# Kernel tuning notes

Hardware: AMD Instinct MI355X
Metric: run time of the kernel (lower is better)

## Reference

```python
import jax, jax.numpy as jnp
import numpy as np

# dims: O=1 templates/chains, L=384 residues, d_pair=d_bias=128, 4 heads x 32
O, L, DP, DB, H, DH = 1, 384, 128, 128, 4, 32
SCALING = 1.0 / np.sqrt(DH)


def _ln(x, g, b):
    # torch nn.LayerNorm over last dim, eps=1e-5, biased variance
    m = jnp.mean(x, axis=-1, keepdims=True)
    v = jnp.mean((x - m) ** 2, axis=-1, keepdims=True)
    return (x - m) * jax.lax.rsqrt(v + 1e-5) * g + b


def setup_inputs() -> dict:
    key = jax.random.key(0)
    ks = jax.random.split(key, 9)

    def w(k, shape, s=0.02):
        return (jax.random.normal(k, shape) * s).astype(jnp.float32)

    return {
        "pair": jax.random.normal(ks[0], (O, L, L, DP), dtype=jnp.float32),
        "bias": jax.random.normal(ks[1], (O, L, L, DB), dtype=jnp.float32),
        "ln_pair_g": jnp.ones((DP,), jnp.float32),
        "ln_pair_b": jnp.zeros((DP,), jnp.float32),
        "ln_bias_g": jnp.ones((DB,), jnp.float32),
        "ln_bias_b": jnp.zeros((DB,), jnp.float32),
        "Wq": w(ks[2], (H * DH, DP)),  # torch Linear weight layout (out, in)
        "Wk": w(ks[3], (H * DH, DP)),
        "Wv": w(ks[4], (H * DH, DP)),
        "Wb": w(ks[5], (H, DB)),
        "Wg": w(ks[6], (H * DH, DP)),
        "bg": jnp.ones((H * DH,), jnp.float32),
        "Wo": w(ks[7], (DP, H * DH)),
        "bo": w(ks[8], (DP,)),
    }


def reference(pair, bias, ln_pair_g, ln_pair_b, ln_bias_g, ln_bias_b,
              Wq, Wk, Wv, Wb, Wg, bg, Wo, bo):
    # is_row=True: swap the two L axes so attention runs along rows
    p = jnp.transpose(pair, (0, 2, 1, 3))   # [O, L, L, DP]
    bsrc = jnp.transpose(bias, (0, 2, 1, 3))  # [O, L, L, DB]

    p = _ln(p, ln_pair_g, ln_pair_b)
    bsrc = _ln(bsrc, ln_bias_g, ln_bias_b)

    q = (p @ Wq.T).reshape(O, L, L, H, DH) * SCALING
    k = (p @ Wk.T).reshape(O, L, L, H, DH) / L
    v = (p @ Wv.T).reshape(O, L, L, H, DH)
    b = bsrc @ Wb.T                         # [O, L, L, H] pairwise bias
    gate = jax.nn.sigmoid(p @ Wg.T + bg)    # [O, L, L, H*DH]

    # attention scores contracted over the non-attended axial dim n and head dim k
    attn = jnp.einsum('bnihk,bnjhk->bijh', q, k) + b
    attn = jax.nn.softmax(attn, axis=2)     # softmax over j (torch dim=-2)

    out = jnp.einsum('bijh,bnjhd->bnihd', attn, v).reshape(O, L, L, H * DH)
    out = (gate * out) @ Wo.T + bo          # [O, L, L, DP]
    return jnp.transpose(out, (0, 2, 1, 3))  # undo is_row permute
```

## Files before the change

kernel.cpp:

```cpp
#include <hip/hip_runtime.h>
#include <hip/hip_bf16.h>

#define L_DIM 384
#define DPC 128
#define NH 4
#define DHD 32
#define HD 128
#define NROWS (L_DIM*L_DIM)
#define NSPLIT 16

typedef __hip_bfloat16 bf16;
typedef __attribute__((ext_vector_type(8))) short bf8_t;
typedef __attribute__((ext_vector_type(4))) short bf4_t;
typedef __attribute__((ext_vector_type(4))) float f4_t;

__device__ __forceinline__ float bf2f(bf16 x){ return __bfloat162float(x); }
__device__ __forceinline__ bf16 f2bf(float x){ return __float2bfloat16(x); }

union bfu8 { bf8_t v; bf16 h[8]; };

__global__ __launch_bounds__(256) void k_prep(
    const float* __restrict__ Wq, const float* __restrict__ Wk, const float* __restrict__ Wv,
    const float* __restrict__ Wg, const float* __restrict__ Wo,
    bf16* __restrict__ Wqp, bf16* __restrict__ Wkp, bf16* __restrict__ Wvp,
    bf16* __restrict__ Wgp, bf16* __restrict__ Wop)
{
  const int o = blockIdx.x * 256 + threadIdx.x;
  const int j = o & 7, lane = (o >> 3) & 63, ks = (o >> 9) & 3, nt = o >> 11;
  const int src = (nt*16 + (lane & 15))*DPC + ks*32 + (lane >> 4)*8 + j;
  Wqp[o] = f2bf(Wq[src]);
  Wkp[o] = f2bf(Wk[src]);
  Wvp[o] = f2bf(Wv[src]);
  Wgp[o] = f2bf(Wg[src]);
  Wop[o] = f2bf(Wo[src]);
}

__global__ __launch_bounds__(256) void k_bias_proj(
    const float* __restrict__ bias, const float* __restrict__ lng, const float* __restrict__ lnb,
    const float* __restrict__ Wb, float* __restrict__ bscore)
{
  const int tid = threadIdx.x;
  const int wave = tid >> 6, lane = tid & 63;
  const int sub = lane >> 4, l16 = lane & 15, c = l16 * 8;
  const int t = blockIdx.x * 16 + wave * 4 + sub;
  const int j = t / L_DIM, i = t % L_DIM;

  const float4 ga = *(const float4*)&lng[c], gb = *(const float4*)&lng[c+4];
  const float4 ba = *(const float4*)&lnb[c], bb = *(const float4*)&lnb[c+4];
  const float4 xa = *(const float4*)&bias[(size_t)t * DPC + c];
  const float4 xb = *(const float4*)&bias[(size_t)t * DPC + c + 4];

  float s  = xa.x+xa.y+xa.z+xa.w + xb.x+xb.y+xb.z+xb.w;
  float ss = xa.x*xa.x+xa.y*xa.y+xa.z*xa.z+xa.w*xa.w
           + xb.x*xb.x+xb.y*xb.y+xb.z*xb.z+xb.w*xb.w;
  #pragma unroll
  for (int off = 8; off; off >>= 1) { s += __shfl_xor(s, off, 64); ss += __shfl_xor(ss, off, 64); }
  const float mean = s * (1.f/128.f);
  const float var  = ss * (1.f/128.f) - mean*mean;
  const float rstd = rsqrtf(var + 1e-5f);
  float y[8];
  y[0]=(xa.x-mean)*rstd*ga.x+ba.x; y[1]=(xa.y-mean)*rstd*ga.y+ba.y;
  y[2]=(xa.z-mean)*rstd*ga.z+ba.z; y[3]=(xa.w-mean)*rstd*ga.w+ba.w;
  y[4]=(xb.x-mean)*rstd*gb.x+bb.x; y[5]=(xb.y-mean)*rstd*gb.y+bb.y;
  y[6]=(xb.z-mean)*rstd*gb.z+bb.z; y[7]=(xb.w-mean)*rstd*gb.w+bb.w;

  float p[4];
  #pragma unroll
  for (int h = 0; h < 4; ++h) {
    const float4 wa = *(const float4*)&Wb[h*DPC + c];
    const float4 wb4 = *(const float4*)&Wb[h*DPC + c + 4];
    p[h] = y[0]*wa.x + y[1]*wa.y + y[2]*wa.z + y[3]*wa.w
         + y[4]*wb4.x + y[5]*wb4.y + y[6]*wb4.z + y[7]*wb4.w;
    #pragma unroll
    for (int off = 8; off; off >>= 1) p[h] += __shfl_xor(p[h], off, 64);
  }
  if (l16 == 0) {
    #pragma unroll
    for (int h = 0; h < 4; ++h)
      bscore[((size_t)h*L_DIM + i)*L_DIM + j] = p[h];
  }
}

__global__ __launch_bounds__(256) void k_pair_proj(
    const float* __restrict__ pair, const float* __restrict__ lng, const float* __restrict__ lnb,
    const bf16* __restrict__ Wqp, const bf16* __restrict__ Wkp, const bf16* __restrict__ Wvp,
    const bf16* __restrict__ Wgp, const float* __restrict__ bg,
    bf16* __restrict__ qf, bf16* __restrict__ kf, bf16* __restrict__ vf, bf16* __restrict__ gatef)
{
  __shared__ __align__(16) bf16 Sh[5120 + 3*4352];
  bf16* AsCT = Sh;
  bf16* Csq  = Sh + 5120;
  bf16* Csk  = Sh + 5120 + 4352;
  bf16* Csg  = Sh + 5120 + 2*4352;
  const int tid = threadIdx.x;
  const int wave = tid >> 6, lane = tid & 63;
  const int n = blockIdx.x / 12, i0 = (blockIdx.x % 12) * 32;
  const int m = lane & 15, q4 = lane >> 4;
  const int rt = wave >> 1, ch = wave & 1;

  {
    const int half = lane >> 5, l32 = lane & 31, c = l32 * 4;
    const float4 g4 = *(const float4*)&lng[c];
    const float4 b4 = *(const float4*)&lnb[c];
    float4 xv[4];
    #pragma unroll
    for (int rr = 0; rr < 4; ++rr) {
      int r = wave*8 + rr*2 + half;
      xv[rr] = *(const float4*)&pair[((size_t)(i0 + r)*L_DIM + n)*DPC + c];
    }
    #pragma unroll
    for (int rr = 0; rr < 4; ++rr) {
      int r = wave*8 + rr*2 + half;
      float s  = xv[rr].x + xv[rr].y + xv[rr].z + xv[rr].w;
      float ss = xv[rr].x*xv[rr].x + xv[rr].y*xv[rr].y + xv[rr].z*xv[rr].z + xv[rr].w*xv[rr].w;
      #pragma unroll
      for (int off = 16; off; off >>= 1) { s += __shfl_xor(s, off, 64); ss += __shfl_xor(ss, off, 64); }
      float mean = s * (1.f/128.f);
      float var  = ss * (1.f/128.f) - mean*mean;
      float rstd = rsqrtf(var + 1e-5f);
      union { bf16 h[4]; bf4_t v; } pk;
      pk.h[0] = f2bf((xv[rr].x-mean)*rstd*g4.x + b4.x);
      pk.h[1] = f2bf((xv[rr].y-mean)*rstd*g4.y + b4.y);
      pk.h[2] = f2bf((xv[rr].z-mean)*rstd*g4.z + b4.z);
      pk.h[3] = f2bf((xv[rr].w-mean)*rstd*g4.w + b4.w);
      *(bf4_t*)&AsCT[r*136 + c] = pk.v;
    }
  }
  __syncthreads();

  bf8_t afr[4];
  #pragma unroll
  for (int ks = 0; ks < 4; ++ks)
    afr[ks] = *(const bf8_t*)&AsCT[(rt*16 + m)*136 + ks*32 + q4*8];

  const bf16* W3[3] = {Wqp, Wkp, Wgp};
  bf16* C3[3] = {Csq, Csk, Csg};
  #pragma unroll
  for (int s3 = 0; s3 < 3; ++s3) {
    const bf16* Wp = W3[s3];
    bf16* Cs = C3[s3];
    #pragma unroll
    for (int ntl = 0; ntl < 4; ++ntl) {
      const int nt = ch*4 + ntl;
      f4_t acc = {0.f, 0.f, 0.f, 0.f};
      #pragma unroll
      for (int ks = 0; ks < 4; ++ks) {
        bf8_t bfr = *(const bf8_t*)&Wp[(nt*4 + ks)*512 + lane*8];
        acc = __builtin_amdgcn_mfma_f32_16x16x32_bf16(afr[ks], bfr, acc, 0, 0, 0);
      }
      const int col = nt*16 + m;
      const float bgv = (s3 == 2) ? bg[col] : 0.f;
      #pragma unroll
      for (int reg = 0; reg < 4; ++reg) {
        float v = acc[reg];
        if (s3 == 2) v = 1.f / (1.f + __expf(-(v + bgv)));
        Cs[(rt*16 + q4*4 + reg)*136 + col] = f2bf(v);
      }
    }
  }
  __syncthreads();

  #pragma unroll
  for (int ntl = 0; ntl < 4; ++ntl) {
    const int nt = ch*4 + ntl;
    f4_t acc = {0.f, 0.f, 0.f, 0.f};
    #pragma unroll
    for (int ks = 0; ks < 4; ++ks) {
      bf8_t bfr = *(const bf8_t*)&Wvp[(nt*4 + ks)*512 + lane*8];
      acc = __builtin_amdgcn_mfma_f32_16x16x32_bf16(afr[ks], bfr, acc, 0, 0, 0);
    }
    const int col = nt*16 + m;
    #pragma unroll
    for (int reg = 0; reg < 4; ++reg)
      AsCT[col*40 + rt*16 + q4*4 + reg] = f2bf(acc[reg]);
  }
  __syncthreads();

  #pragma unroll
  for (int it = 0; it < 2; ++it) {
    int u = tid + it*256;
    {
      int ln = u & 63, dt = (u >> 6) & 1, h = u >> 7;
      bf8_t val = *(const bf8_t*)&AsCT[(h*32 + dt*16 + (ln&15))*40 + (ln>>4)*8];
      size_t dst = ((((size_t)n*NH + h)*12 + (i0>>5))*2 + dt)*512 + (size_t)ln*8;
      *(bf8_t*)&vf[dst] = val;
    }
    {
      int Il = u >> 8, h = (u >> 6) & 3, ln = u & 63;
      int lidx = (Il*16 + (ln&15))*136 + h*32 + (ln>>4)*8;
      size_t dq = ((((size_t)n*NH + h)*24 + (i0>>4) + Il)*64 + ln)*8;
      *(bf8_t*)&qf[dq] = *(const bf8_t*)&Csq[lidx];
      *(bf8_t*)&kf[dq] = *(const bf8_t*)&Csk[lidx];
      size_t dg = ((((size_t)n*24 + (i0>>4) + Il)*NH + h)*64 + ln)*8;
      *(bf8_t*)&gatef[dg] = *(const bf8_t*)&Csg[lidx];
    }
  }
}

__global__ __launch_bounds__(256) void k_qk(
    const bf16* __restrict__ qf, const bf16* __restrict__ kf, float* __restrict__ Spart)
{
  const int tid = threadIdx.x, wave = tid >> 6, lane = tid & 63;
  const int m = lane & 15, q4 = lane >> 4;
  const int b = blockIdx.x;
  const int ks = b / 36, rem = b % 36;
  const int h = rem / 9, t9 = rem % 9;
  const int i0 = (t9/3)*128, j0 = (t9%3)*128;
  const int wr = (wave >> 1)*64, wc = (wave & 1)*64;

  f4_t acc[4][4];
  #pragma unroll
  for (int a = 0; a < 4; ++a)
    #pragma unroll
    for (int c = 0; c < 4; ++c) acc[a][c] = (f4_t){0.f,0.f,0.f,0.f};

  const bf16* qp = qf + (((size_t)(ks*24)*NH + h)*24 + ((i0 + wr) >> 4))*512 + (size_t)lane*8;
  const bf16* kp = kf + (((size_t)(ks*24)*NH + h)*24 + ((j0 + wc) >> 4))*512 + (size_t)lane*8;
  const size_t nstride = (size_t)NH*24*512;

  bf8_t af[4], bfr[4];
  #pragma unroll
  for (int x = 0; x < 4; ++x) {
    af[x]  = *(const bf8_t*)(qp + x*512);
    bfr[x] = *(const bf8_t*)(kp + x*512);
  }
  #pragma unroll 2
  for (int kt = 0; kt < 24; ++kt) {
    bf8_t afn[4], bfn[4];
    if (kt < 23) {
      const bf16* qn = qp + (size_t)(kt+1)*nstride;
      const bf16* kn = kp + (size_t)(kt+1)*nstride;
      #pragma unroll
      for (int x = 0; x < 4; ++x) {
        afn[x] = *(const bf8_t*)(qn + x*512);
        bfn[x] = *(const bf8_t*)(kn + x*512);
      }
    }
    #pragma unroll
    for (int mt = 0; mt < 4; ++mt)
      #pragma unroll
      for (int nt = 0; nt < 4; ++nt)
        acc[mt][nt] = __builtin_amdgcn_mfma_f32_16x16x32_bf16(af[mt], bfr[nt], acc[mt][nt], 0, 0, 0);
    #pragma unroll
    for (int x = 0; x < 4; ++x) { af[x] = afn[x]; bfr[x] = bfn[x]; }
  }
  float* Sp = Spart + (size_t)(ks*NH + h)*L_DIM*L_DIM;
  #pragma unroll
  for (int mt = 0; mt < 4; ++mt)
    #pragma unroll
    for (int nt = 0; nt < 4; ++nt)
      #pragma unroll
      for (int reg = 0; reg < 4; ++reg) {
        int i = i0 + wr + mt*16 + q4*4 + reg;
        int j = j0 + wc + nt*16 + m;
        Sp[(size_t)i*L_DIM + j] = acc[mt][nt][reg];
      }
}

__global__ __launch_bounds__(192) void k_softmax(
    const float* __restrict__ Spart, const float* __restrict__ bscore, bf16* __restrict__ attnf)
{
  const int t = threadIdx.x, wave = t >> 6, lane = t & 63;
  const int h = blockIdx.x / L_DIM, i = blockIdx.x % L_DIM;
  const float sc = 0.17677669529663687f / 384.f;
  const size_t off = ((size_t)h*L_DIM + i)*L_DIM + t*2;

  float ax = 0.f, ay = 0.f;
  #pragma unroll
  for (int ksp = 0; ksp < NSPLIT; ++ksp) {
    float2 p = *(const float2*)&Spart[(size_t)ksp*(NH*L_DIM*L_DIM) + off];
    ax += p.x; ay += p.y;
  }
  const float2 bs = *(const float2*)&bscore[off];
  ax = ax*sc + bs.x;
  ay = ay*sc + bs.y;

  __shared__ float redm[3], reds[3];
  float mx = fmaxf(ax, ay);
  #pragma unroll
  for (int o = 32; o; o >>= 1) mx = fmaxf(mx, __shfl_xor(mx, o, 64));
  if (lane == 0) redm[wave] = mx;
  __syncthreads();
  mx = fmaxf(fmaxf(redm[0], redm[1]), redm[2]);
  float ex = __expf(ax - mx), ey = __expf(ay - mx);
  float sm = ex + ey;
  #pragma unroll
  for (int o = 32; o; o >>= 1) sm += __shfl_xor(sm, o, 64);
  if (lane == 0) reds[wave] = sm;
  __syncthreads();
  const float inv = 1.f / (reds[0] + reds[1] + reds[2]);

  const int j = t*2;
  const int I = i >> 4, mm = i & 15, J = j >> 5, q4 = (j >> 3) & 3, jj = j & 7;
  union { bf16 h2[2]; unsigned u; } pk;
  pk.h2[0] = f2bf(ex * inv);
  pk.h2[1] = f2bf(ey * inv);
  size_t a = ((((size_t)h*24 + I)*12 + J)*64 + q4*16 + mm)*8 + jj;
  *(unsigned*)&attnf[a] = pk.u;
}

__global__ __launch_bounds__(256) void k_pv(
    const bf16* __restrict__ attnf, const bf16* __restrict__ vf, const bf16* __restrict__ gatef,
    bf16* __restrict__ goutf)
{
  __shared__ __align__(16) bf16 Cs2[384*40];
  const int tid = threadIdx.x, wave = tid >> 6, lane = tid & 63;
  const int m = lane & 15, q4 = lane >> 4;
  const int n = blockIdx.x >> 2, h = blockIdx.x & 3;

  bf8_t ugp[6];
  #pragma unroll
  for (int it = 0; it < 6; ++it) {
    int u = tid + it*256;
    int I = u >> 6, ln = u & 63;
    ugp[it] = *(const bf8_t*)&gatef[((((size_t)n*24 + I)*NH + h)*64 + ln)*8];
  }

  f4_t acc[6][2];
  #pragma unroll
  for (int a = 0; a < 6; ++a) { acc[a][0] = (f4_t){0,0,0,0}; acc[a][1] = (f4_t){0,0,0,0}; }

  for (int J = 0; J < 12; ++J) {
    const bf16* vb = vf + (((size_t)(n*NH + h)*12 + J)*2)*512;
    bf8_t b0 = *(const bf8_t*)&vb[lane*8];
    bf8_t b1 = *(const bf8_t*)&vb[512 + lane*8];
    #pragma unroll
    for (int mt = 0; mt < 6; ++mt) {
      const int I = wave*6 + mt;
      bf8_t af = *(const bf8_t*)&attnf[(((size_t)h*24 + I)*12 + J)*512 + (size_t)lane*8];
      acc[mt][0] = __builtin_amdgcn_mfma_f32_16x16x32_bf16(af, b0, acc[mt][0], 0, 0, 0);
      acc[mt][1] = __builtin_amdgcn_mfma_f32_16x16x32_bf16(af, b1, acc[mt][1], 0, 0, 0);
    }
  }
  #pragma unroll
  for (int mt = 0; mt < 6; ++mt)
    #pragma unroll
    for (int dt = 0; dt < 2; ++dt)
      #pragma unroll
      for (int reg = 0; reg < 4; ++reg) {
        int i_loc = 16*(wave*6 + mt) + q4*4 + reg;
        Cs2[i_loc*40 + dt*16 + m] = f2bf(acc[mt][dt][reg]);
      }
  __syncthreads();
  #pragma unroll
  for (int it = 0; it < 6; ++it) {
    int u = tid + it*256;
    int I = u >> 6, ln = u & 63;
    bfu8 uc, ug, uo;
    uc.v = *(const bf8_t*)&Cs2[(I*16 + (ln&15))*40 + (ln>>4)*8];
    ug.v = ugp[it];
    #pragma unroll
    for (int e = 0; e < 8; ++e) uo.h[e] = f2bf(bf2f(uc.h[e]) * bf2f(ug.h[e]));
    size_t gidx = ((((size_t)n*24 + I)*NH + h)*64 + ln)*8;
    *(bf8_t*)&goutf[gidx] = uo.v;
  }
}

__global__ __launch_bounds__(256) void k_out(
    const bf16* __restrict__ goutf, const bf16* __restrict__ Wop, const float* __restrict__ bo,
    float* __restrict__ outp)
{
  __shared__ __align__(16) float Cs[64][132];
  const int tid = threadIdx.x, wave = tid >> 6, lane = tid & 63;
  const int m = lane & 15, q4 = lane >> 4;
  const int n = blockIdx.x / 6, i0 = (blockIdx.x % 6) * 64;

  bf8_t afr[4];
  #pragma unroll
  for (int ks = 0; ks < 4; ++ks)
    afr[ks] = *(const bf8_t*)&goutf[((((size_t)n*24 + (i0>>4) + wave)*NH + ks)*64 + lane)*8];

  #pragma unroll
  for (int nt = 0; nt < 8; ++nt) {
    f4_t acc = {0.f, 0.f, 0.f, 0.f};
    #pragma unroll
    for (int ks = 0; ks < 4; ++ks) {
      bf8_t bfr = *(const bf8_t*)&Wop[(nt*4 + ks)*512 + lane*8];
      acc = __builtin_amdgcn_mfma_f32_16x16x32_bf16(afr[ks], bfr, acc, 0, 0, 0);
    }
    const int col = nt*16 + m;
    const float bov = bo[col];
    #pragma unroll
    for (int reg = 0; reg < 4; ++reg)
      Cs[wave*16 + q4*4 + reg][col] = acc[reg] + bov;
  }
  __syncthreads();
  for (int u = tid; u < 2048; u += 256) {
    int r = u >> 5, c4 = (u & 31) * 4;
    size_t off = ((size_t)(i0 + r)*L_DIM + n)*DPC + c4;
    *(float4*)&outp[off] = *(const float4*)&Cs[r][c4];
  }
}

extern "C" void kernel_launch(void* const* d_in, const int* in_sizes, int n_in,
                              void* d_out, int out_size, void* d_ws, size_t ws_size,
                              hipStream_t stream)
{
  (void)in_sizes; (void)n_in; (void)out_size; (void)ws_size;
  const float* pair = (const float*)d_in[0];
  const float* bias = (const float*)d_in[1];
  const float* lnpg = (const float*)d_in[2];
  const float* lnpb = (const float*)d_in[3];
  const float* lnbg = (const float*)d_in[4];
  const float* lnbb = (const float*)d_in[5];
  const float* Wq   = (const float*)d_in[6];
  const float* Wk   = (const float*)d_in[7];
  const float* Wv   = (const float*)d_in[8];
  const float* Wb   = (const float*)d_in[9];
  const float* Wg   = (const float*)d_in[10];
  const float* bg   = (const float*)d_in[11];
  const float* Wo   = (const float*)d_in[12];
  const float* bo   = (const float*)d_in[13];
  float* outp = (float*)d_out;

  char* ws = (char*)d_ws;
  const size_t SZ = (size_t)NROWS * HD * 2;
  bf16* qfb   = (bf16*)(ws);
  bf16* kfb   = (bf16*)(ws + SZ);
  bf16* vfb   = (bf16*)(ws + 2*SZ);
  bf16* gatef = (bf16*)(ws + 3*SZ);
  float* bscore = (float*)(ws + 4*SZ);
  float* Spart  = (float*)(ws + 4*SZ + (size_t)NH*L_DIM*L_DIM*4);
  bf16*  attnf  = (bf16*)(ws + 4*SZ + (size_t)NH*L_DIM*L_DIM*4 + (size_t)NSPLIT*NH*L_DIM*L_DIM*4);
  char*  wb     = ws + 4*SZ + (size_t)NH*L_DIM*L_DIM*4 + (size_t)NSPLIT*NH*L_DIM*L_DIM*4
                     + (size_t)NH*L_DIM*L_DIM*2;
  bf16* Wqp = (bf16*)(wb);
  bf16* Wkp = (bf16*)(wb + 32768);
  bf16* Wvp = (bf16*)(wb + 65536);
  bf16* Wgp = (bf16*)(wb + 98304);
  bf16* Wop = (bf16*)(wb + 131072);
  bf16* goutf = qfb;

  hipLaunchKernelGGL(k_prep, dim3(64), dim3(256), 0, stream, Wq, Wk, Wv, Wg, Wo,
                     Wqp, Wkp, Wvp, Wgp, Wop);
  hipLaunchKernelGGL(k_bias_proj, dim3(NROWS/16), dim3(256), 0, stream, bias, lnbg, lnbb, Wb, bscore);
  hipLaunchKernelGGL(k_pair_proj, dim3(NROWS/32), dim3(256), 0, stream, pair, lnpg, lnpb,
                     Wqp, Wkp, Wvp, Wgp, bg, qfb, kfb, vfb, gatef);
  hipLaunchKernelGGL(k_qk, dim3(NSPLIT*36), dim3(256), 0, stream, qfb, kfb, Spart);
  hipLaunchKernelGGL(k_softmax, dim3(NH*L_DIM), dim3(192), 0, stream, Spart, bscore, attnf);
  hipLaunchKernelGGL(k_pv, dim3(L_DIM*NH), dim3(256), 0, stream, attnf, vfb, gatef, goutf);
  hipLaunchKernelGGL(k_out, dim3(NROWS/64), dim3(256), 0, stream, goutf, Wop, bo, outp);
}
```

Before: 388.1 us.

## Restructure pair projection into per-wave independent tiles without block barriers

Each wave of the pair projection kernel now owns a 16-row tile with its own shared-memory scratch. It does the layernorm, all four projections and the reformatting into fragment layout without any __syncthreads. The block covers 64 rows instead of 32, halving the grid, and launch bounds request 6 blocks per CU. The aim is to remove block-wide barriers and the serialised staging phases, in exchange for more redundant weight-fragment loads per wave and higher register pressure.

```diff
diff --git a/kernel.cpp b/kernel.cpp
--- a/kernel.cpp
+++ b/kernel.cpp
@@ -81,119 +81,112 @@
   }
 }
 
-__global__ __launch_bounds__(256) void k_pair_proj(
+__global__ __launch_bounds__(256, 6) void k_pair_proj(
     const float* __restrict__ pair, const float* __restrict__ lng, const float* __restrict__ lnb,
     const bf16* __restrict__ Wqp, const bf16* __restrict__ Wkp, const bf16* __restrict__ Wvp,
     const bf16* __restrict__ Wgp, const float* __restrict__ bg,
     bf16* __restrict__ qf, bf16* __restrict__ kf, bf16* __restrict__ vf, bf16* __restrict__ gatef)
 {
-  __shared__ __align__(16) bf16 Sh[5120 + 3*4352];
-  bf16* AsCT = Sh;
-  bf16* Csq  = Sh + 5120;
-  bf16* Csk  = Sh + 5120 + 4352;
-  bf16* Csg  = Sh + 5120 + 2*4352;
+  __shared__ __align__(16) bf16 Sh[4 * 3072];
   const int tid = threadIdx.x;
   const int wave = tid >> 6, lane = tid & 63;
-  const int n = blockIdx.x / 12, i0 = (blockIdx.x % 12) * 32;
+  bf16* WS = Sh + wave * 3072;
+  const int n = blockIdx.x / 6, i6 = blockIdx.x % 6;
+  const int i0g = i6*64 + wave*16;
   const int m = lane & 15, q4 = lane >> 4;
-  const int rt = wave >> 1, ch = wave & 1;
+  const int I = i6*4 + wave;
 
   {
     const int half = lane >> 5, l32 = lane & 31, c = l32 * 4;
     const float4 g4 = *(const float4*)&lng[c];
     const float4 b4 = *(const float4*)&lnb[c];
-    float4 xv[4];
-    #pragma unroll
-    for (int rr = 0; rr < 4; ++rr) {
-      int r = wave*8 + rr*2 + half;
-      xv[rr] = *(const float4*)&pair[((size_t)(i0 + r)*L_DIM + n)*DPC + c];
-    }
-    #pragma unroll
-    for (int rr = 0; rr < 4; ++rr) {
-      int r = wave*8 + rr*2 + half;
+    float4 xv[8];
+    #pragma unroll
+    for (int rr = 0; rr < 8; ++rr)
+      xv[rr] = *(const float4*)&pair[((size_t)(i0g + rr*2 + half)*L_DIM + n)*DPC + c];
+    #pragma unroll
+    for (int rr = 0; rr < 8; ++rr) {
+      const int r = rr*2 + half;
       float s  = xv[rr].x + xv[rr].y + xv[rr].z + xv[rr].w;
       float ss = xv[rr].x*xv[rr].x + xv[rr].y*xv[rr].y + xv[rr].z*xv[rr].z + xv[rr].w*xv[rr].w;
       #pragma unroll
       for (int off = 16; off; off >>= 1) { s += __shfl_xor(s, off, 64); ss += __shfl_xor(ss, off, 64); }
-      float mean = s * (1.f/128.f);
-      float var  = ss * (1.f/128.f) - mean*mean;
-      float rstd = rsqrtf(var + 1e-5f);
+      const float mean = s * (1.f/128.f);
+      const float var  = ss * (1.f/128.f) - mean*mean;
+      const float rstd = rsqrtf(var + 1e-5f);
       union { bf16 h[4]; bf4_t v; } pk;
       pk.h[0] = f2bf((xv[rr].x-mean)*rstd*g4.x + b4.x);
       pk.h[1] = f2bf((xv[rr].y-mean)*rstd*g4.y + b4.y);
       pk.h[2] = f2bf((xv[rr].z-mean)*rstd*g4.z + b4.z);
       pk.h[3] = f2bf((xv[rr].w-mean)*rstd*g4.w + b4.w);
-      *(bf4_t*)&AsCT[r*136 + c] = pk.v;
-    }
-  }
-  __syncthreads();
+      *(bf4_t*)&WS[r*136 + c] = pk.v;
+    }
+  }
 
   bf8_t afr[4];
   #pragma unroll
   for (int ks = 0; ks < 4; ++ks)
-    afr[ks] = *(const bf8_t*)&AsCT[(rt*16 + m)*136 + ks*32 + q4*8];
+    afr[ks] = *(const bf8_t*)&WS[m*136 + ks*32 + q4*8];
 
   const bf16* W3[3] = {Wqp, Wkp, Wgp};
-  bf16* C3[3] = {Csq, Csk, Csg};
   #pragma unroll
   for (int s3 = 0; s3 < 3; ++s3) {
     const bf16* Wp = W3[s3];
-    bf16* Cs = C3[s3];
-    #pragma unroll
-    for (int ntl = 0; ntl < 4; ++ntl) {
-      const int nt = ch*4 + ntl;
-      f4_t acc = {0.f, 0.f, 0.f, 0.f};
+    #pragma unroll
+    for (int h = 0; h < 4; ++h) {
+      f4_t acc0 = {0.f,0.f,0.f,0.f}, acc1 = {0.f,0.f,0.f,0.f};
       #pragma unroll
       for (int ks = 0; ks < 4; ++ks) {
-        bf8_t bfr = *(const bf8_t*)&Wp[(nt*4 + ks)*512 + lane*8];
-        acc = __builtin_amdgcn_mfma_f32_16x16x32_bf16(afr[ks], bfr, acc, 0, 0, 0);
-      }
-      const int col = nt*16 + m;
-      const float bgv = (s3 == 2) ? bg[col] : 0.f;
+        bf8_t b0 = *(const bf8_t*)&Wp[((h*2    )*4 + ks)*512 + lane*8];
+        bf8_t b1 = *(const bf8_t*)&Wp[((h*2 + 1)*4 + ks)*512 + lane*8];
+        acc0 = __builtin_amdgcn_mfma_f32_16x16x32_bf16(afr[ks], b0, acc0, 0, 0, 0);
+        acc1 = __builtin_amdgcn_mfma_f32_16x16x32_bf16(afr[ks], b1, acc1, 0, 0, 0);
+      }
+      if (s3 == 2) {
+        const float bg0 = bg[h*32 + m], bg1 = bg[h*32 + 16 + m];
+        #pragma unroll
+        for (int reg = 0; reg < 4; ++reg) {
+          acc0[reg] = 1.f / (1.f + __expf(-(acc0[reg] + bg0)));
+          acc1[reg] = 1.f / (1.f + __expf(-(acc1[reg] + bg1)));
+        }
+      }
       #pragma unroll
       for (int reg = 0; reg < 4; ++reg) {
-        float v = acc[reg];
-        if (s3 == 2) v = 1.f / (1.f + __expf(-(v + bgv)));
-        Cs[(rt*16 + q4*4 + reg)*136 + col] = f2bf(v);
-      }
-    }
-  }
-  __syncthreads();
-
-  #pragma unroll
-  for (int ntl = 0; ntl < 4; ++ntl) {
-    const int nt = ch*4 + ntl;
-    f4_t acc = {0.f, 0.f, 0.f, 0.f};
+        WS[(q4*4 + reg)*40 + m]      = f2bf(acc0[reg]);
+        WS[(q4*4 + reg)*40 + 16 + m] = f2bf(acc1[reg]);
+      }
+      bf8_t fv = *(const bf8_t*)&WS[m*40 + q4*8];
+      if (s3 == 0)
+        *(bf8_t*)&qf[((((size_t)n*NH + h)*24 + I)*64 + lane)*8] = fv;
+      else if (s3 == 1)
+        *(bf8_t*)&kf[((((size_t)n*NH + h)*24 + I)*64 + lane)*8] = fv;
+      else
+        *(bf8_t*)&gatef[((((size_t)n*24 + I)*NH + h)*64 + lane)*8] = fv;
+    }
+  }
+
+  #pragma unroll
+  for (int nt = 0; nt < 8; ++nt) {
+    f4_t acc = {0.f,0.f,0.f,0.f};
     #pragma unroll
     for (int ks = 0; ks < 4; ++ks) {
       bf8_t bfr = *(const bf8_t*)&Wvp[(nt*4 + ks)*512 + lane*8];
       acc = __builtin_amdgcn_mfma_f32_16x16x32_bf16(afr[ks], bfr, acc, 0, 0, 0);
     }
-    const int col = nt*16 + m;
     #pragma unroll
     for (int reg = 0; reg < 4; ++reg)
-      AsCT[col*40 + rt*16 + q4*4 + reg] = f2bf(acc[reg]);
-  }
-  __syncthreads();
-
-  #pragma unroll
-  for (int it = 0; it < 2; ++it) {
-    int u = tid + it*256;
-    {
-      int ln = u & 63, dt = (u >> 6) & 1, h = u >> 7;
-      bf8_t val = *(const bf8_t*)&AsCT[(h*32 + dt*16 + (ln&15))*40 + (ln>>4)*8];
-      size_t dst = ((((size_t)n*NH + h)*12 + (i0>>5))*2 + dt)*512 + (size_t)ln*8;
-      *(bf8_t*)&vf[dst] = val;
-    }
-    {
-      int Il = u >> 8, h = (u >> 6) & 3, ln = u & 63;
-      int lidx = (Il*16 + (ln&15))*136 + h*32 + (ln>>4)*8;
-      size_t dq = ((((size_t)n*NH + h)*24 + (i0>>4) + Il)*64 + ln)*8;
-      *(bf8_t*)&qf[dq] = *(const bf8_t*)&Csq[lidx];
-      *(bf8_t*)&kf[dq] = *(const bf8_t*)&Csk[lidx];
-      size_t dg = ((((size_t)n*24 + (i0>>4) + Il)*NH + h)*64 + ln)*8;
-      *(bf8_t*)&gatef[dg] = *(const bf8_t*)&Csg[lidx];
-    }
+      WS[(nt*16 + m)*24 + q4*4 + reg] = f2bf(acc[reg]);
+  }
+  const int J  = i6*2 + (wave >> 1);
+  const int wo = (wave & 1) * 32;
+  #pragma unroll
+  for (int st = 0; st < 4; ++st) {
+    const int fid = st*2 + (lane >> 5);
+    const int h = fid >> 1, dt = fid & 1;
+    const int lnl = lane & 31;
+    bf8_t val = *(const bf8_t*)&WS[(h*32 + dt*16 + (lnl & 15))*24 + (lnl >> 4)*8];
+    size_t dst = (((((size_t)n*NH + h)*12 + J)*2 + dt)*64 + (wo + lnl))*8;
+    *(bf8_t*)&vf[dst] = val;
   }
 }
 
@@ -434,7 +427,7 @@
   hipLaunchKernelGGL(k_prep, dim3(64), dim3(256), 0, stream, Wq, Wk, Wv, Wg, Wo,
                      Wqp, Wkp, Wvp, Wgp, Wop);
   hipLaunchKernelGGL(k_bias_proj, dim3(NROWS/16), dim3(256), 0, stream, bias, lnbg, lnbb, Wb, bscore);
-  hipLaunchKernelGGL(k_pair_proj, dim3(NROWS/32), dim3(256), 0, stream, pair, lnpg, lnpb,
+  hipLaunchKernelGGL(k_pair_proj, dim3(NROWS/64), dim3(256), 0, stream, pair, lnpg, lnpb,
                      Wqp, Wkp, Wvp, Wgp, bg, qfb, kfb, vfb, gatef);
   hipLaunchKernelGGL(k_qk, dim3(NSPLIT*36), dim3(256), 0, stream, qfb, kfb, Spart);
   hipLaunchKernelGGL(k_softmax, dim3(NH*L_DIM), dim3(192), 0, stream, Spart, bscore, attnf);
```

After: 392.2 us. Within noise of the previous version (+1.0%).

## Fuse PV attention, gating and output projection into one kernel

Applied to the files above, without the earlier changes.

Merges the attention-times-V kernel and the output projection kernel into a single kernel. Each block now handles one n and a quarter of the i rows across all four heads (one head per wave), stages the PV result in LDS, applies the gate, and runs the Wo projection with bias directly. This drops the bf16 gated-output round trip through global memory and one launch. In exchange each block reads V for all heads and loads more attention data per wave, and the output stores are smaller per-wave float4 chunks.

```diff
diff --git a/kernel.cpp b/kernel.cpp
--- a/kernel.cpp
+++ b/kernel.cpp
@@ -299,22 +299,17 @@
   *(unsigned*)&attnf[a] = pk.u;
 }
 
-__global__ __launch_bounds__(256) void k_pv(
+__global__ __launch_bounds__(256) void k_pv_out(
     const bf16* __restrict__ attnf, const bf16* __restrict__ vf, const bf16* __restrict__ gatef,
-    bf16* __restrict__ goutf)
-{
-  __shared__ __align__(16) bf16 Cs2[384*40];
+    const bf16* __restrict__ Wop, const float* __restrict__ bo, float* __restrict__ outp)
+{
+  __shared__ __align__(16) bf16 G[96*136];
+  __shared__ __align__(16) float CH[4][16*36];
   const int tid = threadIdx.x, wave = tid >> 6, lane = tid & 63;
   const int m = lane & 15, q4 = lane >> 4;
-  const int n = blockIdx.x >> 2, h = blockIdx.x & 3;
-
-  bf8_t ugp[6];
-  #pragma unroll
-  for (int it = 0; it < 6; ++it) {
-    int u = tid + it*256;
-    int I = u >> 6, ln = u & 63;
-    ugp[it] = *(const bf8_t*)&gatef[((((size_t)n*24 + I)*NH + h)*64 + ln)*8];
-  }
+  const int n = blockIdx.x >> 2, iq = blockIdx.x & 3;
+  const int I0 = iq * 6;
+  const int h = wave;
 
   f4_t acc[6][2];
   #pragma unroll
@@ -326,8 +321,7 @@
     bf8_t b1 = *(const bf8_t*)&vb[512 + lane*8];
     #pragma unroll
     for (int mt = 0; mt < 6; ++mt) {
-      const int I = wave*6 + mt;
-      bf8_t af = *(const bf8_t*)&attnf[(((size_t)h*24 + I)*12 + J)*512 + (size_t)lane*8];
+      bf8_t af = *(const bf8_t*)&attnf[(((size_t)h*24 + I0 + mt)*12 + J)*512 + (size_t)lane*8];
       acc[mt][0] = __builtin_amdgcn_mfma_f32_16x16x32_bf16(af, b0, acc[mt][0], 0, 0, 0);
       acc[mt][1] = __builtin_amdgcn_mfma_f32_16x16x32_bf16(af, b1, acc[mt][1], 0, 0, 0);
     }
@@ -337,58 +331,45 @@
     #pragma unroll
     for (int dt = 0; dt < 2; ++dt)
       #pragma unroll
-      for (int reg = 0; reg < 4; ++reg) {
-        int i_loc = 16*(wave*6 + mt) + q4*4 + reg;
-        Cs2[i_loc*40 + dt*16 + m] = f2bf(acc[mt][dt][reg]);
+      for (int reg = 0; reg < 4; ++reg)
+        G[(mt*16 + q4*4 + reg)*136 + h*32 + dt*16 + m] = f2bf(acc[mt][dt][reg]);
+  __syncthreads();
+
+  #pragma unroll
+  for (int t6 = 0; t6 < 6; ++t6) {
+    const int task = wave + t6*4;
+    const int It = task >> 2, ntp = task & 3;
+
+    bf8_t afr[4];
+    #pragma unroll
+    for (int ks = 0; ks < 4; ++ks) {
+      bfu8 ug, uc, uo;
+      uc.v = *(const bf8_t*)&G[(It*16 + m)*136 + ks*32 + q4*8];
+      ug.v = *(const bf8_t*)&gatef[((((size_t)n*24 + I0 + It)*NH + ks)*64 + lane)*8];
+      #pragma unroll
+      for (int e = 0; e < 8; ++e) uo.h[e] = f2bf(bf2f(uc.h[e]) * bf2f(ug.h[e]));
+      afr[ks] = uo.v;
+    }
+    #pragma unroll
+    for (int sub = 0; sub < 2; ++sub) {
+      const int nt = ntp*2 + sub;
+      f4_t acc2 = {0.f, 0.f, 0.f, 0.f};
+      #pragma unroll
+      for (int ks = 0; ks < 4; ++ks) {
+        bf8_t bfr = *(const bf8_t*)&Wop[(nt*4 + ks)*512 + lane*8];
+        acc2 = __builtin_amdgcn_mfma_f32_16x16x32_bf16(afr[ks], bfr, acc2, 0, 0, 0);
       }
-  __syncthreads();
-  #pragma unroll
-  for (int it = 0; it < 6; ++it) {
-    int u = tid + it*256;
-    int I = u >> 6, ln = u & 63;
-    bfu8 uc, ug, uo;
-    uc.v = *(const bf8_t*)&Cs2[(I*16 + (ln&15))*40 + (ln>>4)*8];
-    ug.v = ugp[it];
-    #pragma unroll
-    for (int e = 0; e < 8; ++e) uo.h[e] = f2bf(bf2f(uc.h[e]) * bf2f(ug.h[e]));
-    size_t gidx = ((((size_t)n*24 + I)*NH + h)*64 + ln)*8;
-    *(bf8_t*)&goutf[gidx] = uo.v;
-  }
-}
-
-__global__ __launch_bounds__(256) void k_out(
-    const bf16* __restrict__ goutf, const bf16* __restrict__ Wop, const float* __restrict__ bo,
-    float* __restrict__ outp)
-{
-  __shared__ __align__(16) float Cs[64][132];
-  const int tid = threadIdx.x, wave = tid >> 6, lane = tid & 63;
-  const int m = lane & 15, q4 = lane >> 4;
-  const int n = blockIdx.x / 6, i0 = (blockIdx.x % 6) * 64;
-
-  bf8_t afr[4];
-  #pragma unroll
-  for (int ks = 0; ks < 4; ++ks)
-    afr[ks] = *(const bf8_t*)&goutf[((((size_t)n*24 + (i0>>4) + wave)*NH + ks)*64 + lane)*8];
-
-  #pragma unroll
-  for (int nt = 0; nt < 8; ++nt) {
-    f4_t acc = {0.f, 0.f, 0.f, 0.f};
-    #pragma unroll
-    for (int ks = 0; ks < 4; ++ks) {
-      bf8_t bfr = *(const bf8_t*)&Wop[(nt*4 + ks)*512 + lane*8];
-      acc = __builtin_amdgcn_mfma_f32_16x16x32_bf16(afr[ks], bfr, acc, 0, 0, 0);
-    }
-    const int col = nt*16 + m;
-    const float bov = bo[col];
-    #pragma unroll
-    for (int reg = 0; reg < 4; ++reg)
-      Cs[wave*16 + q4*4 + reg][col] = acc[reg] + bov;
-  }
-  __syncthreads();
-  for (int u = tid; u < 2048; u += 256) {
-    int r = u >> 5, c4 = (u & 31) * 4;
-    size_t off = ((size_t)(i0 + r)*L_DIM + n)*DPC + c4;
-    *(float4*)&outp[off] = *(const float4*)&Cs[r][c4];
+      const float bov = bo[nt*16 + m];
+      #pragma unroll
+      for (int reg = 0; reg < 4; ++reg)
+        CH[wave][(q4*4 + reg)*36 + sub*16 + m] = acc2[reg] + bov;
+    }
+    const int r0 = lane >> 3, c8 = (lane & 7) * 4;
+    float4 v0 = *(const float4*)&CH[wave][r0*36 + c8];
+    float4 v1 = *(const float4*)&CH[wave][(r0 + 8)*36 + c8];
+    const int gr = iq*96 + It*16;
+    *(float4*)&outp[((size_t)(gr + r0     )*L_DIM + n)*DPC + ntp*32 + c8] = v0;
+    *(float4*)&outp[((size_t)(gr + r0 + 8 )*L_DIM + n)*DPC + ntp*32 + c8] = v1;
   }
 }
 
@@ -429,7 +410,6 @@
   bf16* Wvp = (bf16*)(wb + 65536);
   bf16* Wgp = (bf16*)(wb + 98304);
   bf16* Wop = (bf16*)(wb + 131072);
-  bf16* goutf = qfb;
 
   hipLaunchKernelGGL(k_prep, dim3(64), dim3(256), 0, stream, Wq, Wk, Wv, Wg, Wo,
                      Wqp, Wkp, Wvp, Wgp, Wop);
@@ -438,6 +418,6 @@
                      Wqp, Wkp, Wvp, Wgp, bg, qfb, kfb, vfb, gatef);
   hipLaunchKernelGGL(k_qk, dim3(NSPLIT*36), dim3(256), 0, stream, qfb, kfb, Spart);
   hipLaunchKernelGGL(k_softmax, dim3(NH*L_DIM), dim3(192), 0, stream, Spart, bscore, attnf);
-  hipLaunchKernelGGL(k_pv, dim3(L_DIM*NH), dim3(256), 0, stream, attnf, vfb, gatef, goutf);
-  hipLaunchKernelGGL(k_out, dim3(NROWS/64), dim3(256), 0, stream, goutf, Wop, bo, outp);
-}
+  hipLaunchKernelGGL(k_pv_out, dim3(L_DIM*4), dim3(256), 0, stream, attnf, vfb, gatef,
+                     Wop, bo, outp);
+}
```

Result: no change. 394.5 us (+1.6%).
